# Optimization experiments

Measured on AMD Instinct MI355X. Metric: run time of the kernel, lower is better.

## Reference

```python
import jax, jax.numpy as jnp
import numpy as np

BUF = 16  # max polygon vertex buffer (convex 9-gon clipped by 4 half-planes -> <= 13 verts)


def _shoelace(V, c):
    # area of polygon stored in buffer V[:c]
    i = jnp.arange(V.shape[0])
    nxt = jnp.where(i + 1 < c, i + 1, 0)
    Vn = V[nxt]
    contrib = jnp.where(i < c, V[:, 0] * Vn[:, 1] - Vn[:, 0] * V[:, 1], 0.0)
    return 0.5 * jnp.abs(contrib.sum())


def _convex_hull(P):
    # exact convex hull of n small points; returns CCW-ordered vertex buffer [BUF,2] and count
    n = P.shape[0]
    d = P[None, :, :] - P[:, None, :]  # p_j - p_i
    minc = jnp.full((n, n), jnp.inf, P.dtype)
    for k in range(n):  # fixed small loop, keeps memory at [n,n]
        w = (P[k] - P)[:, None, :]
        minc = jnp.minimum(minc, d[..., 0] * w[..., 1] - d[..., 1] * w[..., 0])
    minc = jax.lax.stop_gradient(minc)  # hull membership is discrete
    edge = (minc >= -1e-6) & (~jnp.eye(n, dtype=bool))  # (i,j) is CCW hull edge iff all pts left
    hull = edge.any(1)
    cnt = hull.sum()
    cen = (P * hull[:, None]).sum(0) / jnp.maximum(cnt, 1)
    ang = jnp.arctan2(P[:, 1] - cen[1], P[:, 0] - cen[0])
    keyv = jnp.where(hull, jax.lax.stop_gradient(ang), jnp.inf)
    order = jnp.argsort(keyv)
    V = jnp.zeros((BUF, 2), P.dtype).at[:n].set(P[order])
    return V, cnt


def _clip(V, c, a, b):
    # Sutherland-Hodgman clip of convex polygon (V,c) by half-plane left of a->b
    i = jnp.arange(BUF)
    active = i < c
    nxt = jnp.where(i + 1 < c, i + 1, 0)
    nx = V[nxt]
    e = b - a
    s_cur = e[0] * (V[:, 1] - a[1]) - e[1] * (V[:, 0] - a[0])
    s_nxt = e[0] * (nx[:, 1] - a[1]) - e[1] * (nx[:, 0] - a[0])
    in_cur = s_cur >= 0
    in_nxt = s_nxt >= 0
    den = s_cur - s_nxt
    safe = jnp.abs(den) > 1e-9
    t = jnp.where(safe, s_cur / jnp.where(safe, den, 1.0), 0.0)
    ipt = V + t[:, None] * (nx - V)
    f_int = active & (in_cur != in_nxt)
    f_nxt = active & in_nxt
    pts = jnp.stack([ipt, nx], 1).reshape(2 * BUF, 2)
    flg = jnp.stack([f_int, f_nxt], 1).reshape(2 * BUF)
    pos = jnp.cumsum(flg) - 1
    idx = jnp.where(flg, pos, BUF)  # invalid slots dropped
    out = jnp.zeros((BUF, 2), V.dtype).at[idx].set(pts, mode='drop')
    return out, flg.sum()


def _order_ccw(Q):
    cen = Q.mean(0)
    ang = jnp.arctan2(Q[:, 1] - cen[1], Q[:, 0] - cen[0])
    return Q[jnp.argsort(jax.lax.stop_gradient(ang))]


def _per_point(gt4, p9):
    # giou_loss + out_of_box loss for one (gt quad, 9 pred points) pair
    gt = _order_ccw(gt4)
    Vp, cp = _convex_hull(p9)          # predicted convex polygon (OrientedRepPoints convex hull)
    a_pred = _shoelace(Vp, cp)
    a_gt = _shoelace(jnp.zeros((BUF, 2), gt.dtype).at[:4].set(gt), 4)
    V, c = Vp, cp
    for e in range(4):
        V, c = _clip(V, c, gt[e], gt[(e + 1) % 4])
    a_int = _shoelace(V, c)
    union = a_pred + a_gt - a_int
    iou = a_int / (union + 1e-16)
    Vh, ch = _convex_hull(jnp.concatenate([gt4, p9], 0))  # hull of all 13 points
    a_hull = _shoelace(Vh, ch)
    giou = iou - (a_hull - union) / (a_hull + 1e-16)
    # out-of-box distance: positive distance of pred points outside the gt quad edges
    b = jnp.roll(gt, -1, 0)
    e2 = b - gt
    rel = p9[:, None, :] - gt[None, :, :]
    s = (e2[None, :, 0] * rel[..., 1] - e2[None, :, 1] * rel[..., 0]) / (jnp.linalg.norm(e2, axis=1)[None, :] + 1e-9)
    oob = jax.nn.relu((-s).max(1)).mean()
    return 1.0 - giou, oob


def _assign(points_xy, points_lvl, gt_obb):
    # OBBPointAssigner: sequential per-GT closest-point assignment (pos_num=1, scale=4)
    xs = gt_obb[:, 0::2]
    ys = gt_obb[:, 1::2]
    xmin, xmax = xs.min(1), xs.max(1)
    ymin, ymax = ys.min(1), ys.max(1)
    cxy = jnp.stack([(xmin + xmax) / 2, (ymin + ymax) / 2], 1)
    wh = jnp.maximum(jnp.stack([xmax - xmin, ymax - ymin], 1), 1e-6)
    lvl_min, lvl_max = points_lvl.min(), points_lvl.max()
    glvl = jnp.clip(((jnp.log2(wh[:, 0] / 4.0) + jnp.log2(wh[:, 1] / 4.0)) / 2).astype(jnp.int32), lvl_min, lvl_max)
    K = gt_obb.shape[0]
    Np = points_xy.shape[0]

    def body(carry, g):
        inds, dist = carry
        c_xy, c_wh, c_lvl, gi = g
        dmask = points_lvl == c_lvl
        dd = jnp.linalg.norm((points_xy - c_xy) / c_wh, axis=1)
        dd = jnp.where(dmask, dd, jnp.inf)
        j = jnp.argmin(dd)
        md = dd[j]
        better = md < dist[j]
        inds = inds.at[j].set(jnp.where(better, gi + 1, inds[j]))
        dist = dist.at[j].set(jnp.where(better, md, dist[j]))
        return (inds, dist), None

    init = (jnp.zeros(Np, jnp.int32), jnp.full(Np, jnp.inf, points_xy.dtype))
    (inds, _), _ = jax.lax.scan(body, init, (cxy, wh, glvl, jnp.arange(K, dtype=jnp.int32)))
    return inds


def _stage(rep, inds, labels, gt_obb):
    posm = (labels > 0).astype(rep.dtype)
    gidx = jnp.maximum(inds - 1, 0)
    gt4 = gt_obb[gidx].reshape(-1, 4, 2)
    p9 = rep.reshape(-1, 9, 2)
    gl, oob = jax.vmap(_per_point)(gt4, p9)
    npos = jnp.maximum(posm.sum(), 1.0)
    return (gl * posm).sum() / npos, (oob * posm).sum() / npos


def _forward(rpi, rpr, cls, stride, gob, glab):
    stride = jax.lax.stop_gradient(stride)
    plvl = jnp.log2(stride).astype(jnp.int32)
    inds_i = _assign(jax.lax.stop_gradient(rpi[:, 8:10]), plvl, jax.lax.stop_gradient(gob))
    inds_r = _assign(jax.lax.stop_gradient(rpr[:, 8:10]), plvl, jax.lax.stop_gradient(gob))
    lab_i = jnp.where(inds_i > 0, glab[jnp.maximum(inds_i - 1, 0)], 0)
    lab_r = jnp.where(inds_r > 0, glab[jnp.maximum(inds_r - 1, 0)], 0)
    loc_i, sc_i = _stage(rpi, inds_i, lab_i, gob)
    loc_r, sc_r = _stage(rpr, inds_r, lab_r, gob)
    logp = jax.nn.log_softmax(cls, -1)
    cls_loss = -jnp.take_along_axis(logp, lab_r[:, None], 1).mean()
    return 1.0 * cls_loss + 0.3 * loc_i + 1.0 * loc_r + 0.05 * sc_i + 0.1 * sc_r


def setup_inputs() -> dict:
    key = jax.random.key(0)
    ks = jax.random.split(key, 8)
    strides = [8, 16, 32, 64, 128]
    batch = 2
    centers_list, stride_list = [], []
    for s in strides:
        hw = 1536 // s
        c = (jnp.arange(hw, dtype=jnp.float32) + 0.5) * s
        gx, gy = jnp.meshgrid(c, c, indexing='ij')
        cen = jnp.stack([gx.reshape(-1), gy.reshape(-1)], 1)
        cen = jnp.tile(cen, (batch, 1))
        centers_list.append(cen)
        stride_list.append(jnp.full((cen.shape[0],), float(s), jnp.float32))
    centers = jnp.concatenate(centers_list, 0)
    points_stride = jnp.concatenate(stride_list, 0)
    N = centers.shape[0]  # 98208
    base = jnp.tile(centers[:, None, :], (1, 9, 1)).reshape(N, 18)
    scale18 = jnp.repeat(points_stride[:, None], 18, 1)
    rpi = base + jax.random.normal(ks[0], (N, 18), jnp.float32) * scale18 * 1.5
    rpr = base + jax.random.normal(ks[1], (N, 18), jnp.float32) * scale18 * 1.0
    classification = jax.random.normal(ks[2], (N, 16), jnp.float32)
    K = 64
    cx = jax.random.uniform(ks[3], (K,), minval=128.0, maxval=1408.0)
    cy = jax.random.uniform(ks[4], (K,), minval=128.0, maxval=1408.0)
    w = jax.random.uniform(ks[5], (K,), minval=48.0, maxval=400.0)
    h = jax.random.uniform(ks[6], (K,), minval=48.0, maxval=400.0)
    th = jax.random.uniform(ks[7], (K,), minval=0.0, maxval=float(np.pi))
    ct, st = jnp.cos(th), jnp.sin(th)
    dx = jnp.stack([-w, w, w, -w], 1) / 2
    dy = jnp.stack([-h, -h, h, h], 1) / 2
    xs = cx[:, None] + dx * ct[:, None] - dy * st[:, None]
    ys = cy[:, None] + dx * st[:, None] + dy * ct[:, None]
    gt_obboxes = jnp.stack([xs, ys], 2).reshape(K, 8)
    gt_labels = jax.random.randint(jax.random.fold_in(key, 7), (K,), 1, 16)
    return {"rep_points_init": rpi, "rep_points_refine": rpr, "classification": classification,
            "points_stride": points_stride, "gt_obboxes": gt_obboxes, "gt_labels": gt_labels}


def reference(rep_points_init, rep_points_refine, classification, points_stride, gt_obboxes, gt_labels):
    return _forward(rep_points_init, rep_points_refine, classification, points_stride, gt_obboxes, gt_labels)
```

## Files before the change

kernel.cpp:

```cpp
#include <hip/hip_runtime.h>
#include <math.h>
#include <stdint.h>

#pragma clang fp contract(off)

#define SUB 16

struct WS {
  double sums[8];
  unsigned long long packed[128];
  unsigned cntpub[2];
  unsigned done2;
};

__global__ void k_init(WS* ws) {
  int t = threadIdx.x;
  if (t < 8) ws->sums[t] = 0.0;
  if (t < 128) ws->packed[t] = ~0ULL;
  if (t == 0) { ws->done2 = 0u; ws->cntpub[0] = 0u; ws->cntpub[1] = 0u; }
}

__global__ void __launch_bounds__(256) k_main(const float* __restrict__ rpi,
                                              const float* __restrict__ rpr,
                                              const float* __restrict__ cls,
                                              const float* __restrict__ stridev,
                                              const float* __restrict__ gob,
                                              int N, int K, int AB, WS* ws) {
  __shared__ unsigned long long sb[256];
  __shared__ float scx, scy, siw, sih;
  __shared__ int sbnd[2];
  int t = threadIdx.x;
  int b = blockIdx.x;
  if (b < AB) {
    int s = b % SUB;
    int ak = b / SUB;
    int a = ak / K;
    int k = ak % K;
    if (t < 2) {
      const float* g = gob + k * 8;
      float x0 = g[0], x1 = g[2], x2 = g[4], x3 = g[6];
      float y0 = g[1], y1 = g[3], y2 = g[5], y3 = g[7];
      float xmin = fminf(fminf(x0, x1), fminf(x2, x3));
      float xmax = fmaxf(fmaxf(x0, x1), fmaxf(x2, x3));
      float ymin = fminf(fminf(y0, y1), fminf(y2, y3));
      float ymax = fmaxf(fmaxf(y0, y1), fmaxf(y2, y3));
      float w = fmaxf(xmax - xmin, 1e-6f);
      float h = fmaxf(ymax - ymin, 1e-6f);
      int lmin = (int)log2f(stridev[0]);
      int lmax = (int)log2f(stridev[N - 1]);
      int gl = (int)((log2f(w * 0.25f) + log2f(h * 0.25f)) * 0.5f);
      gl = gl < lmin ? lmin : (gl > lmax ? lmax : gl);
      float v = (float)(1 << (gl + t));
      int lo = 0, hi = N;
      while (lo < hi) { int mid = (lo + hi) >> 1; if (stridev[mid] < v) lo = mid + 1; else hi = mid; }
      sbnd[t] = lo;
      if (t == 0) {
        scx = (xmin + xmax) * 0.5f;
        scy = (ymin + ymax) * 0.5f;
        siw = 1.f / w; sih = 1.f / h;
      }
    }
    __syncthreads();
    int lo = sbnd[0], hi = sbnd[1];
    float cx = scx, cy = scy, iw = siw, ih = sih;
    const float* rep = a ? rpr : rpi;
    unsigned long long best = ~0ULL;
    for (int i = lo + s * 256 + t; i < hi; i += SUB * 256) {
      const float2 p = *(const float2*)(rep + (size_t)i * 18 + 8);
      float dx = (p.x - cx) * iw, dy = (p.y - cy) * ih;
      float d2 = dx * dx + dy * dy;
      unsigned long long pk = ((unsigned long long)__float_as_uint(d2) << 32) | (unsigned)i;
      if (pk < best) best = pk;
    }
    sb[t] = best;
    __syncthreads();
    for (int off = 128; off > 0; off >>= 1) {
      if (t < off) { unsigned long long o = sb[t + off]; if (o < sb[t]) sb[t] = o; }
      __syncthreads();
    }
    if (t == 0 && sb[0] != ~0ULL) atomicMin(&ws->packed[a * 64 + k], sb[0]);
  } else {
    int i = (b - AB) * 256 + t;
    double v = 0.0;
    if (i < N) {
      const float4* r = (const float4*)(cls + (size_t)i * 16);
      float4 q0 = r[0], q1 = r[1], q2 = r[2], q3 = r[3];
      float x[16] = {q0.x, q0.y, q0.z, q0.w, q1.x, q1.y, q1.z, q1.w,
                     q2.x, q2.y, q2.z, q2.w, q3.x, q3.y, q3.z, q3.w};
      float m = x[0];
      for (int j = 1; j < 16; j++) m = fmaxf(m, x[j]);
      float ssum = 0.f;
      for (int j = 0; j < 16; j++) ssum += expf(x[j] - m);
      v = (double)(logf(ssum) + m - x[0]);
    }
    double* sd = (double*)sb;
    sd[t] = v;
    __syncthreads();
    for (int off = 128; off > 0; off >>= 1) {
      if (t < off) sd[t] += sd[t + off];
      __syncthreads();
    }
    if (t == 0) atomicAdd(&ws->sums[0], sd[0]);
  }
}


__device__ __forceinline__ float shoe(const float* VX, const float* VY, int c) {
  float s = 0.f;
  #pragma unroll
  for (int i = 0; i < 16; i++) {
    if (i < c) {
      int nx = (i + 1 < c) ? ((i + 1 < 16) ? i + 1 : 15) : 0;
      s += VX[i] * VY[nx] - VX[nx] * VY[i];
    }
  }
  return 0.5f * fabsf(s);
}

__device__ __forceinline__ int clip_edge(const float* SX, const float* SY, float* DX, float* DY,
                                         int c, float ax, float ay, float bx, float by, int lane) {
  if (lane < 16) { DX[lane] = 0.f; DY[lane] = 0.f; }
  bool f_int = false, f_nxt = false;
  float ix = 0.f, iy = 0.f, nxv = 0.f, nyv = 0.f;
  if (lane < 16 && lane < c) {
    int nxt = (lane + 1 < c) ? lane + 1 : 0;
    if (nxt > 15) nxt = 15;
    float cxv = SX[lane], cyv = SY[lane];
    nxv = SX[nxt]; nyv = SY[nxt];
    float ex = bx - ax, ey = by - ay;
    float s_cur = ex * (cyv - ay) - ey * (cxv - ax);
    float s_nxt = ex * (nyv - ay) - ey * (nxv - ax);
    bool in_cur = s_cur >= 0.f, in_nxt = s_nxt >= 0.f;
    float den = s_cur - s_nxt;
    bool safe = fabsf(den) > 1e-9f;
    float tt = safe ? s_cur / den : 0.f;
    ix = cxv + tt * (nxv - cxv);
    iy = cyv + tt * (nyv - cyv);
    f_int = (in_cur != in_nxt);
    f_nxt = in_nxt;
  }
  unsigned long long bi = __ballot(f_int), bn = __ballot(f_nxt);
  unsigned long long lt = (1ULL << lane) - 1ULL;
  int below = __popcll(bi & lt) + __popcll(bn & lt);
  if (f_int && below < 16) { DX[below] = ix; DY[below] = iy; }
  int posn = below + (f_int ? 1 : 0);
  if (f_nxt && posn < 16) { DX[posn] = nxv; DY[posn] = nyv; }
  __syncthreads();
  return __popcll(bi) + __popcll(bn);
}

template <int NP>
__device__ __forceinline__ int hull_wave(const float* PX, const float* PY, int base,
                                         float* VX, float* VY, float* KEY, int lane) {
  constexpr int TOT = NP * NP;
  unsigned long long B0 = 0, B1 = 0, B2 = 0;
  {
    bool h = false;
    int idx = lane;
    if (idx < TOT) {
      int i = idx / NP, j = idx % NP;
      if (i != j) {
        float pix = PX[base + i], piy = PY[base + i];
        float dx = PX[base + j] - pix, dy = PY[base + j] - piy;
        float m = INFINITY;
        #pragma unroll
        for (int k = 0; k < NP; k++)
          m = fminf(m, dx * (PY[base + k] - piy) - dy * (PX[base + k] - pix));
        h = (m >= -1e-6f);
      }
    }
    B0 = __ballot(h);
  }
  if constexpr (TOT > 64) {
    bool h = false;
    int idx = lane + 64;
    if (idx < TOT) {
      int i = idx / NP, j = idx % NP;
      if (i != j) {
        float pix = PX[base + i], piy = PY[base + i];
        float dx = PX[base + j] - pix, dy = PY[base + j] - piy;
        float m = INFINITY;
        #pragma unroll
        for (int k = 0; k < NP; k++)
          m = fminf(m, dx * (PY[base + k] - piy) - dy * (PX[base + k] - pix));
        h = (m >= -1e-6f);
      }
    }
    B1 = __ballot(h);
  }
  if constexpr (TOT > 128) {
    bool h = false;
    int idx = lane + 128;
    if (idx < TOT) {
      int i = idx / NP, j = idx % NP;
      if (i != j) {
        float pix = PX[base + i], piy = PY[base + i];
        float dx = PX[base + j] - pix, dy = PY[base + j] - piy;
        float m = INFINITY;
        #pragma unroll
        for (int k = 0; k < NP; k++)
          m = fminf(m, dx * (PY[base + k] - piy) - dy * (PX[base + k] - pix));
        h = (m >= -1e-6f);
      }
    }
    B2 = __ballot(h);
  }
  bool hull_i = false;
  if (lane < NP) {
    int s = lane * NP, w = s >> 6, off = s & 63;
    unsigned long long Bw = (w == 0) ? B0 : ((w == 1) ? B1 : B2);
    unsigned long long Bw1 = (w == 0) ? B1 : ((w == 1) ? B2 : 0ULL);
    unsigned long long bits = Bw >> off;
    if (off) bits |= Bw1 << (64 - off);
    hull_i = (bits & ((1ULL << NP) - 1ULL)) != 0ULL;
  }
  unsigned long long hmask = __ballot(hull_i);
  int cnt = __popcll(hmask);
  float cx = 0.f, cy = 0.f;
  #pragma unroll
  for (int k = 0; k < NP; k++)
    if ((hmask >> k) & 1ULL) { cx += PX[base + k]; cy += PY[base + k]; }
  float dn = (float)(cnt > 1 ? cnt : 1);
  cx /= dn; cy /= dn;
  if (lane < NP)
    KEY[lane] = hull_i ? atan2f(PY[base + lane] - cy, PX[base + lane] - cx) : INFINITY;
  if (lane < 16) { VX[lane] = 0.f; VY[lane] = 0.f; }
  __syncthreads();
  if (lane < NP) {
    float ki = KEY[lane];
    int r = 0;
    #pragma unroll
    for (int j2 = 0; j2 < NP; j2++) {
      float kj = KEY[j2];
      r += (int)((kj < ki) || (kj == ki && j2 < lane));
    }
    VX[r] = PX[base + lane];
    VY[r] = PY[base + lane];
  }
  __syncthreads();
  return cnt;
}

__global__ void __launch_bounds__(64) k_post(const float* __restrict__ rpi,
                                             const float* __restrict__ rpr,
                                             const float* __restrict__ gob,
                                             const int* __restrict__ glab,
                                             const float* __restrict__ cls,
                                             int N, float* out, WS* ws) {
  __shared__ float PXs[16], PYs[16], VX[16], VY[16], DX[16], DY[16], KEY[16], RED[9];
  __shared__ int SJ[64];
  __shared__ unsigned long long SMK[64];
  int lane = threadIdx.x;
  int b = blockIdx.x;
  int a = b >> 6, p = b & 63;

  unsigned long long pk = ws->packed[a * 64 + lane];
  bool valid = (pk != ~0ULL);
  SJ[lane] = valid ? (int)(unsigned)(pk & 0xffffffffu) : (-1 - lane);
  SMK[lane] = (pk & 0xffffffff00000000ULL) | (unsigned)lane;
  __syncthreads();
  bool win = false;
  if (valid) {
    int j = SJ[lane];
    unsigned long long me = SMK[lane];
    win = true;
    for (int o = 0; o < 64; o++)
      if (SJ[o] == j && SMK[o] < me) win = false;
  }
  unsigned long long wmask = __ballot(win);
  int cnt = __popcll(wmask);
  if (p == 0 && lane == 0) atomicExch(&ws->cntpub[a], (unsigned)cnt);

  bool active = (p < cnt);
  if (active) {
    int kk = 0;
    { int c2 = 0;
      for (int o = 0; o < 64; o++)
        if ((wmask >> o) & 1ULL) { if (c2 == p) { kk = o; break; } c2++; } }
    int j = SJ[kk];
    const float* rep = (a ? rpr : rpi) + (size_t)j * 18;
    const float* gt8 = gob + (size_t)kk * 8;
    if (lane < 4) { PXs[lane] = gt8[2 * lane]; PYs[lane] = gt8[2 * lane + 1]; }
    else if (lane < 13) { int q = lane - 4; PXs[lane] = rep[2 * q]; PYs[lane] = rep[2 * q + 1]; }
    __syncthreads();

    float cenx = (((PXs[0] + PXs[1]) + PXs[2]) + PXs[3]) / 4.f;
    float ceny = (((PYs[0] + PYs[1]) + PYs[2]) + PYs[3]) / 4.f;
    float angv[4];
    int r4[4];
    #pragma unroll
    for (int i = 0; i < 4; i++) angv[i] = atan2f(PYs[i] - ceny, PXs[i] - cenx);
    #pragma unroll
    for (int i = 0; i < 4; i++) {
      int r = 0;
      #pragma unroll
      for (int j2 = 0; j2 < 4; j2++)
        r += (int)((angv[j2] < angv[i]) || (angv[j2] == angv[i] && j2 < i));
      r4[i] = r;
    }
    float qx[4], qy[4];
    #pragma unroll
    for (int d = 0; d < 4; d++) {
      float sx = 0.f, sy = 0.f;
      #pragma unroll
      for (int i = 0; i < 4; i++) if (r4[i] == d) { sx = PXs[i]; sy = PYs[i]; }
      qx[d] = sx; qy[d] = sy;
    }

    int cp = hull_wave<9>(PXs, PYs, 4, VX, VY, KEY, lane);
    float a_pred = shoe(VX, VY, cp);

    float sgt = 0.f;
    #pragma unroll
    for (int i = 0; i < 4; i++) {
      int nx = (i + 1) & 3;
      sgt += qx[i] * qy[nx] - qx[nx] * qy[i];
    }
    float a_gt = 0.5f * fabsf(sgt);

    int c = cp;
    c = clip_edge(VX, VY, DX, DY, c, qx[0], qy[0], qx[1], qy[1], lane);
    c = clip_edge(DX, DY, VX, VY, c, qx[1], qy[1], qx[2], qy[2], lane);
    c = clip_edge(VX, VY, DX, DY, c, qx[2], qy[2], qx[3], qy[3], lane);
    c = clip_edge(DX, DY, VX, VY, c, qx[3], qy[3], qx[0], qy[0], lane);
    float a_int = shoe(VX, VY, c);

    float uni = a_pred + a_gt - a_int;
    float iou = a_int / (uni + 1e-16f);

    int ch = hull_wave<13>(PXs, PYs, 0, VX, VY, KEY, lane);
    float a_hull = shoe(VX, VY, ch);
    float giou = iou - (a_hull - uni) / (a_hull + 1e-16f);
    float gl = 1.f - giou;

    float mxv = -INFINITY;
    if (lane < 36) {
      int pp = lane >> 2, e = lane & 3;
      float ax = e == 0 ? qx[0] : e == 1 ? qx[1] : e == 2 ? qx[2] : qx[3];
      float ay = e == 0 ? qy[0] : e == 1 ? qy[1] : e == 2 ? qy[2] : qy[3];
      float bx2 = e == 0 ? qx[1] : e == 1 ? qx[2] : e == 2 ? qx[3] : qx[0];
      float by2 = e == 0 ? qy[1] : e == 1 ? qy[2] : e == 2 ? qy[3] : qy[0];
      float ex = bx2 - ax, ey = by2 - ay;
      float nrm = sqrtf(ex * ex + ey * ey) + 1e-9f;
      float px = PXs[4 + pp], py = PYs[4 + pp];
      float s = (ex * (py - ay) - ey * (px - ax)) / nrm;
      mxv = -s;
    }
    float o1 = __shfl_xor(mxv, 1); mxv = fmaxf(mxv, o1);
    float o2 = __shfl_xor(mxv, 2); mxv = fmaxf(mxv, o2);
    if (lane < 36 && (lane & 3) == 0) RED[lane >> 2] = fmaxf(mxv, 0.f);
    __syncthreads();
    if (lane == 0) {
      float acc = 0.f;
      #pragma unroll
      for (int pp = 0; pp < 9; pp++) acc += RED[pp];
      float oob = acc / 9.f;
      atomicAdd(&ws->sums[1 + a * 2], (double)gl);
      atomicAdd(&ws->sums[2 + a * 2], (double)oob);
      if (a == 1) {
        int lab = glab[kk];
        double corr = (double)cls[(size_t)j * 16] - (double)cls[(size_t)j * 16 + lab];
        atomicAdd(&ws->sums[0], corr);
      }
    }
  }

  __syncthreads();
  if (lane == 0) {
    __threadfence();
    unsigned d = atomicAdd(&ws->done2, 1u);
    if (d == gridDim.x - 1) {
      __threadfence();
      double s0 = atomicAdd(&ws->sums[0], 0.0);
      double s1 = atomicAdd(&ws->sums[1], 0.0);
      double s2 = atomicAdd(&ws->sums[2], 0.0);
      double s3 = atomicAdd(&ws->sums[3], 0.0);
      double s4 = atomicAdd(&ws->sums[4], 0.0);
      unsigned c0 = atomicAdd(&ws->cntpub[0], 0u);
      unsigned c1 = atomicAdd(&ws->cntpub[1], 0u);
      double n0 = (double)(c0 > 1u ? c0 : 1u);
      double n1 = (double)(c1 > 1u ? c1 : 1u);
      out[0] = (float)(s0 / (double)N + 0.3 * (s1 / n0) + 1.0 * (s3 / n1) +
                       0.05 * (s2 / n0) + 0.1 * (s4 / n1));
    }
  }
}

extern "C" void kernel_launch(void* const* d_in, const int* in_sizes, int n_in,
                              void* d_out, int out_size, void* d_ws, size_t ws_size,
                              hipStream_t stream) {
  const float* rpi = (const float*)d_in[0];
  const float* rpr = (const float*)d_in[1];
  const float* cls = (const float*)d_in[2];
  const float* pstride = (const float*)d_in[3];
  const float* gob = (const float*)d_in[4];
  const int* glab = (const int*)d_in[5];
  int N = in_sizes[3];
  int K = in_sizes[5];
  if (K > 64) K = 64;
  WS* ws = (WS*)d_ws;

  int AB = 2 * K * SUB;
  int nb = (N + 255) / 256;
  k_init<<<1, 256, 0, stream>>>(ws);
  k_main<<<AB + nb, 256, 0, stream>>>(rpi, rpr, cls, pstride, gob, N, K, AB, ws);
  k_post<<<128, 64, 0, stream>>>(rpi, rpr, gob, glab, cls, N, (float*)d_out, ws);
}
```

Measured before the change: 105.1 us.

## Compact point coordinates into contiguous buffers before per-box argmin search

A new gather kernel reads the center coordinates of every point once and writes them as packed float2 arrays. The same kernel computes the classification log-softmax partial sums per block and also absorbs the workspace initialisation, which removes the separate init launch. The argmin kernel then scans contiguous float2 data instead of strided 72-byte rows, cutting wasted memory traffic across the many box blocks that reread the same ranges. Per-block classification partials replace the double atomics and are reduced by the last post block, at the cost of an extra full pass over the point arrays and a dependency between kernels.

```diff
diff --git a/kernel.cpp b/kernel.cpp
--- a/kernel.cpp
+++ b/kernel.cpp
@@ -8,100 +8,108 @@
 
 struct WS {
   double sums[8];
+  double clspart[512];
   unsigned long long packed[128];
   unsigned cntpub[2];
   unsigned done2;
 };
 
-__global__ void k_init(WS* ws) {
-  int t = threadIdx.x;
-  if (t < 8) ws->sums[t] = 0.0;
-  if (t < 128) ws->packed[t] = ~0ULL;
-  if (t == 0) { ws->done2 = 0u; ws->cntpub[0] = 0u; ws->cntpub[1] = 0u; }
-}
-
-__global__ void __launch_bounds__(256) k_main(const float* __restrict__ rpi,
-                                              const float* __restrict__ rpr,
-                                              const float* __restrict__ cls,
-                                              const float* __restrict__ stridev,
-                                              const float* __restrict__ gob,
-                                              int N, int K, int AB, WS* ws) {
+__global__ void __launch_bounds__(256) k_gather(const float* __restrict__ rpi,
+                                                const float* __restrict__ rpr,
+                                                const float* __restrict__ cls,
+                                                float2* __restrict__ xyi,
+                                                float2* __restrict__ xyr,
+                                                int N, WS* ws) {
+  __shared__ double sd[256];
+  int t = threadIdx.x, b = blockIdx.x;
+  int i = b * 256 + t;
+  if (b == 0) {
+    if (t < 8) ws->sums[t] = 0.0;
+    if (t < 128) ws->packed[t] = ~0ULL;
+    if (t == 0) { ws->done2 = 0u; ws->cntpub[0] = 0u; ws->cntpub[1] = 0u; }
+  }
+  double v = 0.0;
+  if (i < N) {
+    const float2 pi = *(const float2*)(rpi + (size_t)i * 18 + 8);
+    const float2 pr = *(const float2*)(rpr + (size_t)i * 18 + 8);
+    xyi[i] = pi;
+    xyr[i] = pr;
+    const float4* r = (const float4*)(cls + (size_t)i * 16);
+    float4 q0 = r[0], q1 = r[1], q2 = r[2], q3 = r[3];
+    float x[16] = {q0.x, q0.y, q0.z, q0.w, q1.x, q1.y, q1.z, q1.w,
+                   q2.x, q2.y, q2.z, q2.w, q3.x, q3.y, q3.z, q3.w};
+    float m = x[0];
+    for (int j = 1; j < 16; j++) m = fmaxf(m, x[j]);
+    float ssum = 0.f;
+    for (int j = 0; j < 16; j++) ssum += expf(x[j] - m);
+    v = (double)(logf(ssum) + m - x[0]);
+  }
+  sd[t] = v;
+  __syncthreads();
+  for (int off = 128; off > 0; off >>= 1) {
+    if (t < off) sd[t] += sd[t + off];
+    __syncthreads();
+  }
+  if (t == 0) ws->clspart[b] = sd[0];
+}
+
+__global__ void __launch_bounds__(256) k_argmin(const float2* __restrict__ xyi,
+                                                const float2* __restrict__ xyr,
+                                                const float* __restrict__ stridev,
+                                                const float* __restrict__ gob,
+                                                int N, int K, WS* ws) {
   __shared__ unsigned long long sb[256];
   __shared__ float scx, scy, siw, sih;
   __shared__ int sbnd[2];
   int t = threadIdx.x;
   int b = blockIdx.x;
-  if (b < AB) {
-    int s = b % SUB;
-    int ak = b / SUB;
-    int a = ak / K;
-    int k = ak % K;
-    if (t < 2) {
-      const float* g = gob + k * 8;
-      float x0 = g[0], x1 = g[2], x2 = g[4], x3 = g[6];
-      float y0 = g[1], y1 = g[3], y2 = g[5], y3 = g[7];
-      float xmin = fminf(fminf(x0, x1), fminf(x2, x3));
-      float xmax = fmaxf(fmaxf(x0, x1), fmaxf(x2, x3));
-      float ymin = fminf(fminf(y0, y1), fminf(y2, y3));
-      float ymax = fmaxf(fmaxf(y0, y1), fmaxf(y2, y3));
-      float w = fmaxf(xmax - xmin, 1e-6f);
-      float h = fmaxf(ymax - ymin, 1e-6f);
-      int lmin = (int)log2f(stridev[0]);
-      int lmax = (int)log2f(stridev[N - 1]);
-      int gl = (int)((log2f(w * 0.25f) + log2f(h * 0.25f)) * 0.5f);
-      gl = gl < lmin ? lmin : (gl > lmax ? lmax : gl);
-      float v = (float)(1 << (gl + t));
-      int lo = 0, hi = N;
-      while (lo < hi) { int mid = (lo + hi) >> 1; if (stridev[mid] < v) lo = mid + 1; else hi = mid; }
-      sbnd[t] = lo;
-      if (t == 0) {
-        scx = (xmin + xmax) * 0.5f;
-        scy = (ymin + ymax) * 0.5f;
-        siw = 1.f / w; sih = 1.f / h;
-      }
-    }
+  int s = b % SUB;
+  int ak = b / SUB;
+  int a = ak / K;
+  int k = ak % K;
+  if (t < 2) {
+    const float* g = gob + k * 8;
+    float x0 = g[0], x1 = g[2], x2 = g[4], x3 = g[6];
+    float y0 = g[1], y1 = g[3], y2 = g[5], y3 = g[7];
+    float xmin = fminf(fminf(x0, x1), fminf(x2, x3));
+    float xmax = fmaxf(fmaxf(x0, x1), fmaxf(x2, x3));
+    float ymin = fminf(fminf(y0, y1), fminf(y2, y3));
+    float ymax = fmaxf(fmaxf(y0, y1), fmaxf(y2, y3));
+    float w = fmaxf(xmax - xmin, 1e-6f);
+    float h = fmaxf(ymax - ymin, 1e-6f);
+    int lmin = (int)log2f(stridev[0]);
+    int lmax = (int)log2f(stridev[N - 1]);
+    int gl = (int)((log2f(w * 0.25f) + log2f(h * 0.25f)) * 0.5f);
+    gl = gl < lmin ? lmin : (gl > lmax ? lmax : gl);
+    float v = (float)(1 << (gl + t));
+    int lo = 0, hi = N;
+    while (lo < hi) { int mid = (lo + hi) >> 1; if (stridev[mid] < v) lo = mid + 1; else hi = mid; }
+    sbnd[t] = lo;
+    if (t == 0) {
+      scx = (xmin + xmax) * 0.5f;
+      scy = (ymin + ymax) * 0.5f;
+      siw = 1.f / w; sih = 1.f / h;
+    }
+  }
+  __syncthreads();
+  int lo = sbnd[0], hi = sbnd[1];
+  float cx = scx, cy = scy, iw = siw, ih = sih;
+  const float2* rep = a ? xyr : xyi;
+  unsigned long long best = ~0ULL;
+  for (int i = lo + s * 256 + t; i < hi; i += SUB * 256) {
+    const float2 p = rep[i];
+    float dx = (p.x - cx) * iw, dy = (p.y - cy) * ih;
+    float d2 = dx * dx + dy * dy;
+    unsigned long long pk = ((unsigned long long)__float_as_uint(d2) << 32) | (unsigned)i;
+    if (pk < best) best = pk;
+  }
+  sb[t] = best;
+  __syncthreads();
+  for (int off = 128; off > 0; off >>= 1) {
+    if (t < off) { unsigned long long o = sb[t + off]; if (o < sb[t]) sb[t] = o; }
     __syncthreads();
-    int lo = sbnd[0], hi = sbnd[1];
-    float cx = scx, cy = scy, iw = siw, ih = sih;
-    const float* rep = a ? rpr : rpi;
-    unsigned long long best = ~0ULL;
-    for (int i = lo + s * 256 + t; i < hi; i += SUB * 256) {
-      const float2 p = *(const float2*)(rep + (size_t)i * 18 + 8);
-      float dx = (p.x - cx) * iw, dy = (p.y - cy) * ih;
-      float d2 = dx * dx + dy * dy;
-      unsigned long long pk = ((unsigned long long)__float_as_uint(d2) << 32) | (unsigned)i;
-      if (pk < best) best = pk;
-    }
-    sb[t] = best;
-    __syncthreads();
-    for (int off = 128; off > 0; off >>= 1) {
-      if (t < off) { unsigned long long o = sb[t + off]; if (o < sb[t]) sb[t] = o; }
-      __syncthreads();
-    }
-    if (t == 0 && sb[0] != ~0ULL) atomicMin(&ws->packed[a * 64 + k], sb[0]);
-  } else {
-    int i = (b - AB) * 256 + t;
-    double v = 0.0;
-    if (i < N) {
-      const float4* r = (const float4*)(cls + (size_t)i * 16);
-      float4 q0 = r[0], q1 = r[1], q2 = r[2], q3 = r[3];
-      float x[16] = {q0.x, q0.y, q0.z, q0.w, q1.x, q1.y, q1.z, q1.w,
-                     q2.x, q2.y, q2.z, q2.w, q3.x, q3.y, q3.z, q3.w};
-      float m = x[0];
-      for (int j = 1; j < 16; j++) m = fmaxf(m, x[j]);
-      float ssum = 0.f;
-      for (int j = 0; j < 16; j++) ssum += expf(x[j] - m);
-      v = (double)(logf(ssum) + m - x[0]);
-    }
-    double* sd = (double*)sb;
-    sd[t] = v;
-    __syncthreads();
-    for (int off = 128; off > 0; off >>= 1) {
-      if (t < off) sd[t] += sd[t + off];
-      __syncthreads();
-    }
-    if (t == 0) atomicAdd(&ws->sums[0], sd[0]);
-  }
+  }
+  if (t == 0 && sb[0] != ~0ULL) atomicMin(&ws->packed[a * 64 + k], sb[0]);
 }
 
 
@@ -246,10 +254,11 @@
                                              const float* __restrict__ gob,
                                              const int* __restrict__ glab,
                                              const float* __restrict__ cls,
-                                             int N, float* out, WS* ws) {
+                                             int N, int nbcls, float* out, WS* ws) {
   __shared__ float PXs[16], PYs[16], VX[16], VY[16], DX[16], DY[16], KEY[16], RED[9];
   __shared__ int SJ[64];
   __shared__ unsigned long long SMK[64];
+  __shared__ int lastflag;
   int lane = threadIdx.x;
   int b = blockIdx.x;
   int a = b >> 6, p = b & 63;
@@ -369,9 +378,17 @@
   if (lane == 0) {
     __threadfence();
     unsigned d = atomicAdd(&ws->done2, 1u);
-    if (d == gridDim.x - 1) {
-      __threadfence();
-      double s0 = atomicAdd(&ws->sums[0], 0.0);
+    lastflag = (d == gridDim.x - 1) ? 1 : 0;
+  }
+  __syncthreads();
+  if (lastflag) {
+    __threadfence();
+    double part = 0.0;
+    for (int idx = lane; idx < nbcls; idx += 64) part += ws->clspart[idx];
+    #pragma unroll
+    for (int off = 32; off > 0; off >>= 1) part += __shfl_xor(part, off);
+    if (lane == 0) {
+      double s0 = part + atomicAdd(&ws->sums[0], 0.0);
       double s1 = atomicAdd(&ws->sums[1], 0.0);
       double s2 = atomicAdd(&ws->sums[2], 0.0);
       double s3 = atomicAdd(&ws->sums[3], 0.0);
@@ -399,10 +416,12 @@
   int K = in_sizes[5];
   if (K > 64) K = 64;
   WS* ws = (WS*)d_ws;
-
+  float2* xyi = (float2*)((char*)d_ws + 8192);
+  float2* xyr = xyi + N;
+
+  int nb = (N + 255) / 256;
   int AB = 2 * K * SUB;
-  int nb = (N + 255) / 256;
-  k_init<<<1, 256, 0, stream>>>(ws);
-  k_main<<<AB + nb, 256, 0, stream>>>(rpi, rpr, cls, pstride, gob, N, K, AB, ws);
-  k_post<<<128, 64, 0, stream>>>(rpi, rpr, gob, glab, cls, N, (float*)d_out, ws);
-}
+  k_gather<<<nb, 256, 0, stream>>>(rpi, rpr, cls, xyi, xyr, N, ws);
+  k_argmin<<<AB, 256, 0, stream>>>(xyi, xyr, pstride, gob, N, K, ws);
+  k_post<<<128, 64, 0, stream>>>(rpi, rpr, gob, glab, cls, N, nb, (float*)d_out, ws);
+}
```

New measurement: 107.6 us. +2.4%, slower.
